# Kernel tuning notes

Hardware: AMD Instinct MI355X
Metric: run time of the kernel (lower is better)

Reference implementation:

```python
import jax, jax.numpy as jnp
import numpy as np

B, S, HIDDEN = 2, 2048, 2048
N_HEADS, N_KV_HEADS = 32, 8
HEAD_DIM = HIDDEN // N_HEADS          # 64
HALF = HEAD_DIM // 2                  # 32
N_REP = N_HEADS // N_KV_HEADS         # 4
NEG_INF = -1e9


def setup_inputs() -> dict:
    key = jax.random.key(0)
    ks = jax.random.split(key, 5)
    scale = 0.02
    x = jax.random.normal(ks[0], (B, S, HIDDEN), dtype=jnp.float32)
    wq = jax.random.normal(ks[1], (HIDDEN, N_HEADS * HEAD_DIM), dtype=jnp.float32) * scale
    wk = jax.random.normal(ks[2], (HIDDEN, N_KV_HEADS * HEAD_DIM), dtype=jnp.float32) * scale
    wv = jax.random.normal(ks[3], (HIDDEN, N_KV_HEADS * HEAD_DIM), dtype=jnp.float32) * scale
    wo = jax.random.normal(ks[4], (HIDDEN, HIDDEN), dtype=jnp.float32) * scale
    # Llama rotary frequencies: theta = 10000^{-2i/d}, angles = pos * theta
    inv_freq = 1.0 / (10000.0 ** (np.arange(0, HEAD_DIM, 2, dtype=np.float32) / HEAD_DIM))
    angles = np.arange(S, dtype=np.float32)[:, None] * inv_freq[None, :]  # [S, HALF]
    freqs_cos = jnp.asarray(np.cos(angles), dtype=jnp.float32)
    freqs_sin = jnp.asarray(np.sin(angles), dtype=jnp.float32)
    mask = jnp.tril(jnp.ones((S, S), dtype=bool))[None, None]  # causal [1,1,S,S]
    return {"x": x, "wq": wq, "wk": wk, "wv": wv, "wo": wo,
            "freqs_cos": freqs_cos, "freqs_sin": freqs_sin, "mask": mask}


def _apply_rope(t, cos, sin):
    # t: [B, S, H, HEAD_DIM]; cos/sin: [S, HALF] -> broadcast [1, S, 1, HALF]
    tr, ti = t[..., ::2], t[..., 1::2]           # real/imag halves (interleaved pairing)
    c = cos[None, :, None, :]
    s = sin[None, :, None, :]
    out_r = tr * c - ti * s
    out_i = tr * s + ti * c
    out = jnp.stack([out_r, out_i], axis=-1)     # [B,S,H,HALF,2]
    return out.reshape(t.shape)                  # re-interleave


def reference(x, wq, wk, wv, wo, freqs_cos, freqs_sin, mask):
    b, s, _ = x.shape
    xq = (x @ wq).reshape(b, s, N_HEADS, HEAD_DIM)
    xk = (x @ wk).reshape(b, s, N_KV_HEADS, HEAD_DIM)
    xv = (x @ wv).reshape(b, s, N_KV_HEADS, HEAD_DIM)
    xq = _apply_rope(xq, freqs_cos, freqs_sin)
    xk = _apply_rope(xk, freqs_cos, freqs_sin)
    # repeat_kv: interleave-repeat kv heads to match query heads
    xk = jnp.repeat(xk, N_REP, axis=2)           # [B,S,N_HEADS,HEAD_DIM]
    xv = jnp.repeat(xv, N_REP, axis=2)
    q = jnp.transpose(xq, (0, 2, 1, 3))          # [B,H,S,D]
    k = jnp.transpose(xk, (0, 2, 1, 3))
    v = jnp.transpose(xv, (0, 2, 1, 3))
    attn = jnp.einsum('bhqd,bhkd->bhqk', q, k) / jnp.sqrt(jnp.float32(HEAD_DIM))
    attn = attn + (1.0 - mask.astype(attn.dtype)) * NEG_INF  # keras Softmax masking
    attn = jax.nn.softmax(attn, axis=-1)
    out = jnp.einsum('bhqk,bhkd->bhqd', attn, v)
    out = jnp.transpose(out, (0, 2, 1, 3)).reshape(b, s, HIDDEN)
    return out @ wo
```

## Files before the change

kernel.cpp:

```cpp
#include <hip/hip_runtime.h>
#include <cstdint>
#include <cstddef>

#define S_LEN 2048
#define HIDDEN 2048
#define NH 32
#define NKV 8
#define HD 64
#define QKV_W 3072

typedef __bf16 bf16;
typedef __bf16 bf16x8 __attribute__((ext_vector_type(8)));
typedef __bf16 bf16x4 __attribute__((ext_vector_type(4)));
typedef float f32x4 __attribute__((ext_vector_type(4)));
typedef float f32x16 __attribute__((ext_vector_type(16)));

__device__ __forceinline__ void async16(const bf16* g, bf16* l) {
  __builtin_amdgcn_global_load_lds((const __attribute__((address_space(1))) void*)g,
                                   (__attribute__((address_space(3))) void*)l, 16, 0, 0);
}

__global__ void cast_x_kernel(const float* __restrict__ in, bf16* __restrict__ out, int n4) {
  int i = blockIdx.x * blockDim.x + threadIdx.x;
  if (i >= n4) return;
  f32x4 v = ((const f32x4*)in)[i];
  bf16x4 o;
  o[0] = (bf16)v[0]; o[1] = (bf16)v[1]; o[2] = (bf16)v[2]; o[3] = (bf16)v[3];
  ((bf16x4*)out)[i] = o;
}

__global__ void transpose_cast_kernel(const float* __restrict__ in, bf16* __restrict__ out,
                                      int K, int N) {
  __shared__ float tile[32][33];
  const int n0 = blockIdx.x * 32, k0 = blockIdx.y * 32;
  const int tx = threadIdx.x, ty = threadIdx.y;
#pragma unroll
  for (int i = 0; i < 32; i += 8)
    tile[ty + i][tx] = in[(size_t)(k0 + ty + i) * N + n0 + tx];
  __syncthreads();
#pragma unroll
  for (int i = 0; i < 32; i += 8)
    out[(size_t)(n0 + ty + i) * K + k0 + tx] = (bf16)tile[tx][ty + i];
}

template <int MODE>
__global__ __launch_bounds__(256) void gemm_bt_kernel(const bf16* __restrict__ A,
                                                      const bf16* __restrict__ Bt,
                                                      void* __restrict__ Cv,
                                                      int M, int N, int K,
                                                      const float* __restrict__ cosp,
                                                      const float* __restrict__ sinp,
                                                      bf16* __restrict__ vtp) {
  __shared__ bf16 Al[128 * 64];
  __shared__ bf16 Bl[128 * 64];
  const int tid = threadIdx.x;
  const int lane = tid & 63, w = tid >> 6;
  const int quad = lane >> 4, l16 = lane & 15;
  const int m0 = blockIdx.y * 128, n0 = blockIdx.x * 128;
  const int wm = (w >> 1) * 64, wn = (w & 1) * 64;
  f32x4 acc[4][4] = {};
  const int srow = tid >> 3;
  const int scol = (((tid & 7) ^ (srow & 7))) * 8;
  const bf16* Ab = A + (size_t)(m0 + srow) * K + scol;
  const bf16* Bb = Bt + (size_t)(n0 + srow) * K + scol;
  bf16* alp = Al + tid * 8;
  bf16* blp = Bl + tid * 8;
  for (int kt = 0; kt < K; kt += 64) {
    __syncthreads();
#pragma unroll
    for (int j = 0; j < 4; ++j) {
      async16(Ab + (size_t)(32 * j) * K + kt, alp + j * 2048);
      async16(Bb + (size_t)(32 * j) * K + kt, blp + j * 2048);
    }
    __syncthreads();
    bf16x8 a[4][2], b[4][2];
#pragma unroll
    for (int mi = 0; mi < 4; ++mi)
#pragma unroll
      for (int kk = 0; kk < 2; ++kk)
        a[mi][kk] = *(const bf16x8*)(Al + (wm + mi * 16 + l16) * 64 +
                                     (((kk << 2) | quad) ^ (l16 & 7)) * 8);
#pragma unroll
    for (int ni = 0; ni < 4; ++ni)
#pragma unroll
      for (int kk = 0; kk < 2; ++kk)
        b[ni][kk] = *(const bf16x8*)(Bl + (wn + ni * 16 + l16) * 64 +
                                     (((kk << 2) | quad) ^ (l16 & 7)) * 8);
#pragma unroll
    for (int kk = 0; kk < 2; ++kk)
#pragma unroll
      for (int mi = 0; mi < 4; ++mi)
#pragma unroll
        for (int ni = 0; ni < 4; ++ni)
          acc[mi][ni] = __builtin_amdgcn_mfma_f32_16x16x32_bf16(a[mi][kk], b[ni][kk],
                                                                acc[mi][ni], 0, 0, 0);
  }
  if (MODE == 0) {
#pragma unroll
    for (int mi = 0; mi < 4; ++mi)
#pragma unroll
      for (int ni = 0; ni < 4; ++ni)
#pragma unroll
        for (int i = 0; i < 4; ++i) {
          const int row = m0 + wm + mi * 16 + quad * 4 + i;
          const int col = n0 + wn + ni * 16 + l16;
          ((float*)Cv)[(size_t)row * N + col] = acc[mi][ni][i];
        }
  } else if (n0 < 2560) {
#pragma unroll
    for (int mi = 0; mi < 4; ++mi)
#pragma unroll
      for (int ni = 0; ni < 4; ++ni)
#pragma unroll
        for (int i = 0; i < 4; ++i) {
          const int row = m0 + wm + mi * 16 + quad * 4 + i;
          const int col = n0 + wn + ni * 16 + l16;
          const float v = acc[mi][ni][i];
          const float p = __shfl_xor(v, 1);
          const int st = row & (S_LEN - 1);
          const int j = (col & 63) >> 1;
          const float cc = cosp[st * 32 + j], ss = sinp[st * 32 + j];
          const float ov = (l16 & 1) ? (p * ss + v * cc) : (v * cc - p * ss);
          ((bf16*)Cv)[(size_t)row * N + col] = (bf16)ov;
        }
  } else {
#pragma unroll
    for (int mi = 0; mi < 4; ++mi)
#pragma unroll
      for (int ni = 0; ni < 4; ++ni) {
        const int col = n0 + wn + ni * 16 + l16;
        const int c = col - 2560;
        const int row0 = m0 + wm + mi * 16 + quad * 4;
        const int batch = row0 >> 11, st0 = row0 & (S_LEN - 1);
        bf16x4 d4;
#pragma unroll
        for (int i = 0; i < 4; ++i) d4[i] = (bf16)acc[mi][ni][i];
        *(bf16x4*)&vtp[((size_t)batch * 512 + c) * S_LEN + st0] = d4;
      }
  }
}

__global__ __launch_bounds__(256) void attn_kernel(const bf16* __restrict__ qkv,
                                                   const bf16* __restrict__ vt,
                                                   bf16* __restrict__ out) {
  __shared__ bf16 Kl[64 * 72];
  __shared__ bf16 Vl[64 * 72];
  __shared__ bf16 Pl[4][32 * 72];
  const int tid = threadIdx.x;
  const int lane = tid & 63, w = tid >> 6;
  const int l32 = lane & 31, half = lane >> 5;
  const int qt = blockIdx.x, h = blockIdx.y, b = blockIdx.z;
  const int kvh = h >> 2;
  const bf16* Kbase = qkv + ((size_t)b * S_LEN) * QKV_W + 2048 + kvh * HD;
  const bf16* vtb = vt + ((size_t)b * 512 + kvh * 64) * S_LEN;
  const int sr = tid >> 3, sc = (tid & 7) * 8;
  bf16* pw = Pl[w];

  const int Q0 = qt * 128;
  const int qw = Q0 + w * 32;
  const int q = qw + l32;
  const bf16* Qrow = qkv + ((size_t)b * S_LEN + q) * QKV_W + h * HD;
  bf16x8 bq[4];
#pragma unroll
  for (int dc = 0; dc < 4; ++dc) bq[dc] = *(const bf16x8*)(Qrow + dc * 16 + half * 8);
  float l_acc = 0.f;
  f32x16 o0 = {}, o1 = {};
  const int ntiles = 2 * qt + 2;
  for (int t = 0; t < ntiles; ++t) {
    const int kt = t * 64;
    __syncthreads();
    *(bf16x8*)&Kl[sr * 72 + sc]        = *(const bf16x8*)(Kbase + (size_t)(kt + sr) * QKV_W + sc);
    *(bf16x8*)&Kl[(sr + 32) * 72 + sc] = *(const bf16x8*)(Kbase + (size_t)(kt + sr + 32) * QKV_W + sc);
    *(bf16x8*)&Vl[sr * 72 + sc]        = *(const bf16x8*)(vtb + (size_t)sr * S_LEN + kt + sc);
    *(bf16x8*)&Vl[(sr + 32) * 72 + sc] = *(const bf16x8*)(vtb + (size_t)(sr + 32) * S_LEN + kt + sc);
    __syncthreads();
    if (kt > qw + 31) continue;
    f32x16 s0 = {}, s1 = {};
#pragma unroll
    for (int dc = 0; dc < 4; ++dc) {
      const bf16x8 ak0 = *(const bf16x8*)&Kl[l32 * 72 + dc * 16 + half * 8];
      const bf16x8 ak1 = *(const bf16x8*)&Kl[(32 + l32) * 72 + dc * 16 + half * 8];
      s0 = __builtin_amdgcn_mfma_f32_32x32x16_bf16(ak0, bq[dc], s0, 0, 0, 0);
      s1 = __builtin_amdgcn_mfma_f32_32x32x16_bf16(ak1, bq[dc], s1, 0, 0, 0);
    }
    const bool needMask = (kt + 63 > qw);
#pragma unroll
    for (int ks = 0; ks < 2; ++ks) {
      const f32x16 sv = ks ? s1 : s0;
#pragma unroll
      for (int r = 0; r < 4; ++r) {
        bf16x4 pv;
#pragma unroll
        for (int c = 0; c < 4; ++c) {
          float p = __expf(fmaf(sv[r * 4 + c], 0.125f, -4.0f));
          const int key = kt + ks * 32 + 8 * r + 4 * half + c;
          if (needMask && key > q) p = 0.f;
          l_acc += p;
          pv[c] = (bf16)p;
        }
        *(bf16x4*)&pw[l32 * 72 + ks * 32 + 8 * r + 4 * half] = pv;
      }
    }
    bf16x8 bp[4];
#pragma unroll
    for (int kc = 0; kc < 4; ++kc) bp[kc] = *(const bf16x8*)&pw[l32 * 72 + kc * 16 + half * 8];
#pragma unroll
    for (int kc = 0; kc < 4; ++kc) {
      const bf16x8 av0 = *(const bf16x8*)&Vl[l32 * 72 + kc * 16 + half * 8];
      const bf16x8 av1 = *(const bf16x8*)&Vl[(32 + l32) * 72 + kc * 16 + half * 8];
      o0 = __builtin_amdgcn_mfma_f32_32x32x16_bf16(av0, bp[kc], o0, 0, 0, 0);
      o1 = __builtin_amdgcn_mfma_f32_32x32x16_bf16(av1, bp[kc], o1, 0, 0, 0);
    }
  }
  const float lt = l_acc + __shfl_xor(l_acc, 32);
  const float rl = 1.0f / lt;
  bf16* orow = out + ((size_t)b * S_LEN + q) * HIDDEN + h * HD;
#pragma unroll
  for (int dsub = 0; dsub < 2; ++dsub) {
    const f32x16 ov = dsub ? o1 : o0;
#pragma unroll
    for (int r = 0; r < 4; ++r) {
      bf16x4 d4;
#pragma unroll
      for (int c = 0; c < 4; ++c) d4[c] = (bf16)(ov[r * 4 + c] * rl);
      *(bf16x4*)(orow + dsub * 32 + 8 * r + 4 * half) = d4;
    }
  }
}

extern "C" void kernel_launch(void* const* d_in, const int* in_sizes, int n_in,
                              void* d_out, int out_size, void* d_ws, size_t ws_size,
                              hipStream_t stream) {
  const float* x = (const float*)d_in[0];
  const float* wq = (const float*)d_in[1];
  const float* wk = (const float*)d_in[2];
  const float* wv = (const float*)d_in[3];
  const float* wo = (const float*)d_in[4];
  const float* fc = (const float*)d_in[5];
  const float* fs = (const float*)d_in[6];

  char* ws = (char*)d_ws;
  bf16* xb   = (bf16*)(ws);
  bf16* wT   = (bf16*)(ws + 16777216);
  bf16* woT  = (bf16*)(ws + 29360128);
  bf16* qkv  = (bf16*)(ws + 37748736);
  bf16* aout = (bf16*)(ws + 62914560);
  bf16* vt   = (bf16*)(ws + 79691776);

  cast_x_kernel<<<8192, 256, 0, stream>>>(x, xb, 2097152);
  transpose_cast_kernel<<<dim3(64, 64), dim3(32, 8), 0, stream>>>(wq, wT, 2048, 2048);
  transpose_cast_kernel<<<dim3(16, 64), dim3(32, 8), 0, stream>>>(wk, wT + (size_t)2048 * 2048, 2048, 512);
  transpose_cast_kernel<<<dim3(16, 64), dim3(32, 8), 0, stream>>>(wv, wT + (size_t)2560 * 2048, 2048, 512);
  transpose_cast_kernel<<<dim3(64, 64), dim3(32, 8), 0, stream>>>(wo, woT, 2048, 2048);

  gemm_bt_kernel<1><<<dim3(24, 32), 256, 0, stream>>>(xb, wT, (void*)qkv, 4096, 3072, 2048, fc, fs, vt);
  attn_kernel<<<dim3(16, 32, 2), 256, 0, stream>>>(qkv, vt, aout);
  gemm_bt_kernel<0><<<dim3(16, 32), 256, 0, stream>>>(aout, woT, d_out, 4096, 2048, 2048, nullptr, nullptr, nullptr);
}
```

Before: 379.9 us.

## Split RoPE and V transpose into separate kernels; restructure attention inner loop

RoPE and the V transpose move out of the QKV GEMM epilogue into two standalone kernels, so the GEMM writes plain bf16. The attention kernel now loads K/V tiles asynchronously into XOR-swizzled LDS instead of padded rows. It passes P to the PV MFMA through cross-lane shuffles rather than an LDS round-trip, and uses exp2 with prescaled constants. Query tiles are remapped to a flattened, staggered grid to balance causal work. The extra kernels add launches and a full read-write pass over QKV, in exchange for a simpler epilogue and a leaner attention loop.

```diff
diff --git a/kernel.cpp b/kernel.cpp
--- a/kernel.cpp
+++ b/kernel.cpp
@@ -12,8 +12,10 @@
 typedef __bf16 bf16;
 typedef __bf16 bf16x8 __attribute__((ext_vector_type(8)));
 typedef __bf16 bf16x4 __attribute__((ext_vector_type(4)));
+typedef __bf16 bf16x2 __attribute__((ext_vector_type(2)));
 typedef float f32x4 __attribute__((ext_vector_type(4)));
 typedef float f32x16 __attribute__((ext_vector_type(16)));
+typedef unsigned int u32;
 
 __device__ __forceinline__ void async16(const bf16* g, bf16* l) {
   __builtin_amdgcn_global_load_lds((const __attribute__((address_space(1))) void*)g,
@@ -43,14 +45,44 @@
     out[(size_t)(n0 + ty + i) * K + k0 + tx] = (bf16)tile[tx][ty + i];
 }
 
-template <int MODE>
+__global__ void vt_kernel(const bf16* __restrict__ qkv, bf16* __restrict__ vt) {
+  __shared__ bf16 tile[32][33];
+  const int s0 = blockIdx.x * 32, c0 = blockIdx.y * 32, b = blockIdx.z;
+  const int tx = threadIdx.x, ty = threadIdx.y;
+#pragma unroll
+  for (int i = 0; i < 32; i += 8)
+    tile[ty + i][tx] = qkv[((size_t)b * S_LEN + s0 + ty + i) * QKV_W + 2560 + c0 + tx];
+  __syncthreads();
+#pragma unroll
+  for (int i = 0; i < 32; i += 8)
+    vt[((size_t)b * 512 + c0 + ty + i) * S_LEN + s0 + tx] = tile[tx][ty + i];
+}
+
+__global__ void rope_kernel(bf16* __restrict__ qkv, const float* __restrict__ cosp,
+                            const float* __restrict__ sinp, int total) {
+  int idx = blockIdx.x * blockDim.x + threadIdx.x;
+  if (idx >= total) return;
+  const int row = idx / 320;
+  const int col = (idx - row * 320) * 8;
+  const int s = row & (S_LEN - 1);
+  const int j0 = (col >> 1) & 31;
+  bf16* ptr = qkv + (size_t)row * QKV_W + col;
+  bf16x8 v = *(bf16x8*)ptr;
+#pragma unroll
+  for (int u = 0; u < 4; ++u) {
+    const float tr = (float)v[2 * u], ti = (float)v[2 * u + 1];
+    const float c = cosp[s * 32 + j0 + u], sn = sinp[s * 32 + j0 + u];
+    v[2 * u] = (bf16)(tr * c - ti * sn);
+    v[2 * u + 1] = (bf16)(tr * sn + ti * c);
+  }
+  *(bf16x8*)ptr = v;
+}
+
+template <int OUT_BF16>
 __global__ __launch_bounds__(256) void gemm_bt_kernel(const bf16* __restrict__ A,
                                                       const bf16* __restrict__ Bt,
                                                       void* __restrict__ Cv,
-                                                      int M, int N, int K,
-                                                      const float* __restrict__ cosp,
-                                                      const float* __restrict__ sinp,
-                                                      bf16* __restrict__ vtp) {
+                                                      int M, int N, int K) {
   __shared__ bf16 Al[128 * 64];
   __shared__ bf16 Bl[128 * 64];
   const int tid = threadIdx.x;
@@ -95,66 +127,40 @@
           acc[mi][ni] = __builtin_amdgcn_mfma_f32_16x16x32_bf16(a[mi][kk], b[ni][kk],
                                                                 acc[mi][ni], 0, 0, 0);
   }
-  if (MODE == 0) {
-#pragma unroll
-    for (int mi = 0; mi < 4; ++mi)
-#pragma unroll
-      for (int ni = 0; ni < 4; ++ni)
-#pragma unroll
-        for (int i = 0; i < 4; ++i) {
-          const int row = m0 + wm + mi * 16 + quad * 4 + i;
-          const int col = n0 + wn + ni * 16 + l16;
+#pragma unroll
+  for (int mi = 0; mi < 4; ++mi)
+#pragma unroll
+    for (int ni = 0; ni < 4; ++ni)
+#pragma unroll
+      for (int i = 0; i < 4; ++i) {
+        const int row = m0 + wm + mi * 16 + quad * 4 + i;
+        const int col = n0 + wn + ni * 16 + l16;
+        if (OUT_BF16)
+          ((bf16*)Cv)[(size_t)row * N + col] = (bf16)acc[mi][ni][i];
+        else
           ((float*)Cv)[(size_t)row * N + col] = acc[mi][ni][i];
-        }
-  } else if (n0 < 2560) {
-#pragma unroll
-    for (int mi = 0; mi < 4; ++mi)
-#pragma unroll
-      for (int ni = 0; ni < 4; ++ni)
-#pragma unroll
-        for (int i = 0; i < 4; ++i) {
-          const int row = m0 + wm + mi * 16 + quad * 4 + i;
-          const int col = n0 + wn + ni * 16 + l16;
-          const float v = acc[mi][ni][i];
-          const float p = __shfl_xor(v, 1);
-          const int st = row & (S_LEN - 1);
-          const int j = (col & 63) >> 1;
-          const float cc = cosp[st * 32 + j], ss = sinp[st * 32 + j];
-          const float ov = (l16 & 1) ? (p * ss + v * cc) : (v * cc - p * ss);
-          ((bf16*)Cv)[(size_t)row * N + col] = (bf16)ov;
-        }
-  } else {
-#pragma unroll
-    for (int mi = 0; mi < 4; ++mi)
-#pragma unroll
-      for (int ni = 0; ni < 4; ++ni) {
-        const int col = n0 + wn + ni * 16 + l16;
-        const int c = col - 2560;
-        const int row0 = m0 + wm + mi * 16 + quad * 4;
-        const int batch = row0 >> 11, st0 = row0 & (S_LEN - 1);
-        bf16x4 d4;
-#pragma unroll
-        for (int i = 0; i < 4; ++i) d4[i] = (bf16)acc[mi][ni][i];
-        *(bf16x4*)&vtp[((size_t)batch * 512 + c) * S_LEN + st0] = d4;
       }
-  }
 }
 
 __global__ __launch_bounds__(256) void attn_kernel(const bf16* __restrict__ qkv,
                                                    const bf16* __restrict__ vt,
                                                    bf16* __restrict__ out) {
-  __shared__ bf16 Kl[64 * 72];
-  __shared__ bf16 Vl[64 * 72];
-  __shared__ bf16 Pl[4][32 * 72];
+  __shared__ bf16 Kl[64 * 64];
+  __shared__ bf16 Vl[64 * 64];
   const int tid = threadIdx.x;
   const int lane = tid & 63, w = tid >> 6;
   const int l32 = lane & 31, half = lane >> 5;
-  const int qt = blockIdx.x, h = blockIdx.y, b = blockIdx.z;
+  const int f = blockIdx.x;
+  const int b = f >> 9, h = (f >> 4) & 31;
+  const int qt = ((f & 15) + (f >> 6)) & 15;
   const int kvh = h >> 2;
   const bf16* Kbase = qkv + ((size_t)b * S_LEN) * QKV_W + 2048 + kvh * HD;
   const bf16* vtb = vt + ((size_t)b * 512 + kvh * 64) * S_LEN;
-  const int sr = tid >> 3, sc = (tid & 7) * 8;
-  bf16* pw = Pl[w];
+  const int sr = tid >> 3;
+  const int sc = ((tid & 7) ^ (sr & 7)) * 8;
+  bf16* kl_dst = Kl + tid * 8;
+  bf16* vl_dst = Vl + tid * 8;
+  const int xr = l32 & 7;
 
   const int Q0 = qt * 128;
   const int qw = Q0 + w * 32;
@@ -165,51 +171,74 @@
   for (int dc = 0; dc < 4; ++dc) bq[dc] = *(const bf16x8*)(Qrow + dc * 16 + half * 8);
   float l_acc = 0.f;
   f32x16 o0 = {}, o1 = {};
+  const float C1 = 0.125f * 1.44269504f, C2 = -4.0f * 1.44269504f;
   const int ntiles = 2 * qt + 2;
   for (int t = 0; t < ntiles; ++t) {
     const int kt = t * 64;
     __syncthreads();
-    *(bf16x8*)&Kl[sr * 72 + sc]        = *(const bf16x8*)(Kbase + (size_t)(kt + sr) * QKV_W + sc);
-    *(bf16x8*)&Kl[(sr + 32) * 72 + sc] = *(const bf16x8*)(Kbase + (size_t)(kt + sr + 32) * QKV_W + sc);
-    *(bf16x8*)&Vl[sr * 72 + sc]        = *(const bf16x8*)(vtb + (size_t)sr * S_LEN + kt + sc);
-    *(bf16x8*)&Vl[(sr + 32) * 72 + sc] = *(const bf16x8*)(vtb + (size_t)(sr + 32) * S_LEN + kt + sc);
+    async16(Kbase + (size_t)(kt + sr) * QKV_W + sc, kl_dst);
+    async16(Kbase + (size_t)(kt + sr + 32) * QKV_W + sc, kl_dst + 2048);
+    async16(vtb + (size_t)sr * S_LEN + kt + sc, vl_dst);
+    async16(vtb + (size_t)(sr + 32) * S_LEN + kt + sc, vl_dst + 2048);
     __syncthreads();
     if (kt > qw + 31) continue;
     f32x16 s0 = {}, s1 = {};
 #pragma unroll
     for (int dc = 0; dc < 4; ++dc) {
-      const bf16x8 ak0 = *(const bf16x8*)&Kl[l32 * 72 + dc * 16 + half * 8];
-      const bf16x8 ak1 = *(const bf16x8*)&Kl[(32 + l32) * 72 + dc * 16 + half * 8];
+      const int ch = (((dc << 1) | half) ^ xr) * 8;
+      const bf16x8 ak0 = *(const bf16x8*)&Kl[l32 * 64 + ch];
+      const bf16x8 ak1 = *(const bf16x8*)&Kl[(32 + l32) * 64 + ch];
       s0 = __builtin_amdgcn_mfma_f32_32x32x16_bf16(ak0, bq[dc], s0, 0, 0, 0);
       s1 = __builtin_amdgcn_mfma_f32_32x32x16_bf16(ak1, bq[dc], s1, 0, 0, 0);
     }
-    const bool needMask = (kt + 63 > qw);
-#pragma unroll
-    for (int ks = 0; ks < 2; ++ks) {
-      const f32x16 sv = ks ? s1 : s0;
-#pragma unroll
-      for (int r = 0; r < 4; ++r) {
-        bf16x4 pv;
-#pragma unroll
-        for (int c = 0; c < 4; ++c) {
-          float p = __expf(fmaf(sv[r * 4 + c], 0.125f, -4.0f));
-          const int key = kt + ks * 32 + 8 * r + 4 * half + c;
-          if (needMask && key > q) p = 0.f;
-          l_acc += p;
-          pv[c] = (bf16)p;
+    u32 P[16];
+    if (kt + 63 <= qw) {
+#pragma unroll
+      for (int ks = 0; ks < 2; ++ks) {
+        const f32x16 sv = ks ? s1 : s0;
+#pragma unroll
+        for (int u = 0; u < 8; ++u) {
+          const float p0 = exp2f(fmaf(sv[2 * u], C1, C2));
+          const float p1 = exp2f(fmaf(sv[2 * u + 1], C1, C2));
+          l_acc += p0 + p1;
+          union { bf16x2 h2; u32 u32v; } cv;
+          cv.h2[0] = (bf16)p0; cv.h2[1] = (bf16)p1;
+          P[ks * 8 + u] = cv.u32v;
         }
-        *(bf16x4*)&pw[l32 * 72 + ks * 32 + 8 * r + 4 * half] = pv;
       }
-    }
-    bf16x8 bp[4];
-#pragma unroll
-    for (int kc = 0; kc < 4; ++kc) bp[kc] = *(const bf16x8*)&pw[l32 * 72 + kc * 16 + half * 8];
-#pragma unroll
-    for (int kc = 0; kc < 4; ++kc) {
-      const bf16x8 av0 = *(const bf16x8*)&Vl[l32 * 72 + kc * 16 + half * 8];
-      const bf16x8 av1 = *(const bf16x8*)&Vl[(32 + l32) * 72 + kc * 16 + half * 8];
-      o0 = __builtin_amdgcn_mfma_f32_32x32x16_bf16(av0, bp[kc], o0, 0, 0, 0);
-      o1 = __builtin_amdgcn_mfma_f32_32x32x16_bf16(av1, bp[kc], o1, 0, 0, 0);
+    } else {
+#pragma unroll
+      for (int ks = 0; ks < 2; ++ks) {
+        const f32x16 sv = ks ? s1 : s0;
+#pragma unroll
+        for (int u = 0; u < 8; ++u) {
+          const int key0 = kt + ks * 32 + 8 * (u >> 1) + 2 * (u & 1) + 4 * half;
+          float p0 = exp2f(fmaf(sv[2 * u], C1, C2));
+          float p1 = exp2f(fmaf(sv[2 * u + 1], C1, C2));
+          if (key0 > q) p0 = 0.f;
+          if (key0 + 1 > q) p1 = 0.f;
+          l_acc += p0 + p1;
+          union { bf16x2 h2; u32 u32v; } cv;
+          cv.h2[0] = (bf16)p0; cv.h2[1] = (bf16)p1;
+          P[ks * 8 + u] = cv.u32v;
+        }
+      }
+    }
+#pragma unroll
+    for (int g = 0; g < 4; ++g) {
+      const u32 a0 = P[4 * g], a1 = P[4 * g + 1], a2 = P[4 * g + 2], a3 = P[4 * g + 3];
+      const u32 x0 = __shfl_xor((int)a0, 32), x1 = __shfl_xor((int)a1, 32);
+      const u32 x2 = __shfl_xor((int)a2, 32), x3 = __shfl_xor((int)a3, 32);
+      union { u32 uu[4]; bf16x8 v; } F;
+      F.uu[0] = half ? x2 : a0;
+      F.uu[1] = half ? x3 : a1;
+      F.uu[2] = half ? a2 : x0;
+      F.uu[3] = half ? a3 : x1;
+      const int ch = (((g << 1) | half) ^ xr) * 8;
+      const bf16x8 av0 = *(const bf16x8*)&Vl[l32 * 64 + ch];
+      const bf16x8 av1 = *(const bf16x8*)&Vl[(32 + l32) * 64 + ch];
+      o0 = __builtin_amdgcn_mfma_f32_32x32x16_bf16(av0, F.v, o0, 0, 0, 0);
+      o1 = __builtin_amdgcn_mfma_f32_32x32x16_bf16(av1, F.v, o1, 0, 0, 0);
     }
   }
   const float lt = l_acc + __shfl_xor(l_acc, 32);
@@ -253,7 +282,9 @@
   transpose_cast_kernel<<<dim3(16, 64), dim3(32, 8), 0, stream>>>(wv, wT + (size_t)2560 * 2048, 2048, 512);
   transpose_cast_kernel<<<dim3(64, 64), dim3(32, 8), 0, stream>>>(wo, woT, 2048, 2048);
 
-  gemm_bt_kernel<1><<<dim3(24, 32), 256, 0, stream>>>(xb, wT, (void*)qkv, 4096, 3072, 2048, fc, fs, vt);
-  attn_kernel<<<dim3(16, 32, 2), 256, 0, stream>>>(qkv, vt, aout);
-  gemm_bt_kernel<0><<<dim3(16, 32), 256, 0, stream>>>(aout, woT, d_out, 4096, 2048, 2048, nullptr, nullptr, nullptr);
-}
+  gemm_bt_kernel<1><<<dim3(24, 32), 256, 0, stream>>>(xb, wT, (void*)qkv, 4096, 3072, 2048);
+  rope_kernel<<<5120, 256, 0, stream>>>(qkv, fc, fs, 1310720);
+  vt_kernel<<<dim3(64, 16, 2), dim3(32, 8), 0, stream>>>(qkv, vt);
+  attn_kernel<<<1024, 256, 0, stream>>>(qkv, vt, aout);
+  gemm_bt_kernel<0><<<dim3(16, 32), 256, 0, stream>>>(aout, woT, d_out, 4096, 2048, 2048);
+}
```

Result: faster. 362.8 us (-4.5%).
